# Kernel optimization log

Hardware: AMD Instinct MI355X
Metric: run time of the kernel (lower is better)

Reference implementation:

```python
import jax, jax.numpy as jnp
import numpy as np

D = 1024      # model_dim
H = 16        # num_heads
HD = D // H   # head_size
B = 4
S = 2048


def setup_inputs() -> dict:
    key = jax.random.key(0)
    ks = jax.random.split(key, 6)
    sc = 1.0 / np.sqrt(D)
    embedded = jax.random.normal(ks[0], (B, S, D), dtype=jnp.float32)
    # Per-head projection weights stacked: [H, D, HD] (nn.Linear, bias=False)
    Wq = jax.random.normal(ks[1], (H, D, HD), dtype=jnp.float32) * sc
    Wk = jax.random.normal(ks[2], (H, D, HD), dtype=jnp.float32) * sc
    Wv = jax.random.normal(ks[3], (H, D, HD), dtype=jnp.float32) * sc
    # Output projection nn.Linear(D, D) with bias
    Wo = jax.random.normal(ks[4], (D, D), dtype=jnp.float32) * sc
    bo = jax.random.normal(ks[5], (D,), dtype=jnp.float32) * sc
    return {"embedded": embedded, "Wq": Wq, "Wk": Wk, "Wv": Wv, "Wo": Wo, "bo": bo}


def reference(embedded, Wq, Wk, Wv, Wo, bo):
    # q,k,v: [B, H, S, HD]
    q = jnp.einsum('bsd,hde->bhse', embedded, Wq)
    k = jnp.einsum('bsd,hde->bhse', embedded, Wk)
    v = jnp.einsum('bsd,hde->bhse', embedded, Wv)
    scores = jnp.einsum('bhse,bhte->bhst', q, k) / jnp.sqrt(jnp.float32(HD))
    causal = jnp.tril(jnp.ones((S, S), dtype=bool))  # [S, S]
    scores = jnp.where(causal, scores, -jnp.inf)
    attn = jax.nn.softmax(scores, axis=-1)
    ctx = jnp.einsum('bhst,bhte->bhse', attn, v)  # [B, H, S, HD]
    # concat heads -> [B, S, D]
    concat = jnp.transpose(ctx, (0, 2, 1, 3)).reshape(B, S, D)
    # dropout=0.0 -> identity
    return concat @ Wo.T + bo
```

## Files before the change

### kernel.cpp

```cpp
#include <hip/hip_runtime.h>
#include <hip/hip_bf16.h>
#include <stdint.h>
#include <stddef.h>

typedef __bf16 bf16;
typedef __bf16 bf16x4 __attribute__((ext_vector_type(4)));
typedef __bf16 bf16x8 __attribute__((ext_vector_type(8)));
typedef float f32x4 __attribute__((ext_vector_type(4)));
typedef float f32x16 __attribute__((ext_vector_type(16)));


__device__ __forceinline__ void gload16(const void* g, void* lds) {
  __builtin_amdgcn_global_load_lds(
      (const __attribute__((address_space(1))) unsigned int*)(uintptr_t)g,
      (__attribute__((address_space(3))) unsigned int*)(unsigned int)(uintptr_t)lds,
      16, 0, 0);
}

__device__ __forceinline__ bf16x8 lds_read8(const bf16* base, int row, int slot) {
  const char* p = (const char*)base + row * 128 + ((slot ^ (row & 7)) << 4);
  return *(const bf16x8*)p;
}

__device__ __forceinline__ float f3max(float a, float b, float c) {
  return fmaxf(fmaxf(a, b), c);
}


__global__ void k_cvt_embed(const float* __restrict__ src, bf16* __restrict__ dst) {
  int i = blockIdx.x * blockDim.x + threadIdx.x;
  const float4* s4 = (const float4*)src;
  float4 a = s4[2 * i], b = s4[2 * i + 1];
  bf16x8 v;
  v[0] = (bf16)a.x; v[1] = (bf16)a.y; v[2] = (bf16)a.z; v[3] = (bf16)a.w;
  v[4] = (bf16)b.x; v[5] = (bf16)b.y; v[6] = (bf16)b.z; v[7] = (bf16)b.w;
  ((bf16x8*)dst)[i] = v;
}


__global__ void k_cvt_w(const float* __restrict__ Wq, const float* __restrict__ Wk,
                        const float* __restrict__ Wv, const float* __restrict__ Wo,
                        bf16* __restrict__ WT, bf16* __restrict__ WoB) {
  int i = blockIdx.x * blockDim.x + threadIdx.x;
  if (i < 16 * 192 * 1024) {
    int h = i / (192 * 1024);
    int rem = i - h * (192 * 1024);
    int r = rem >> 10;
    int d = rem & 1023;
    const float* W = (r < 64) ? Wq : (r < 128 ? Wk : Wv);
    int e = r & 63;
    WT[i] = (bf16)W[h * 65536 + d * 64 + e];
  } else {
    int j = i - 16 * 192 * 1024;
    WoB[j] = (bf16)Wo[j];
  }
}


__launch_bounds__(256, 2)
__global__ void k_qkv(const bf16* __restrict__ E, const bf16* __restrict__ WT,
                      bf16* __restrict__ Qo, bf16* __restrict__ Ko, bf16* __restrict__ Vt) {
  __shared__ __align__(16) bf16 As[128 * 64];
  __shared__ __align__(16) bf16 Bs[192 * 64];
  const int h = blockIdx.y;
  const int m0 = blockIdx.x * 128;
  const int tid = threadIdx.x;
  const int w = tid >> 6, lane = tid & 63;
  const int wm = w >> 1, wn = w & 1;
  const int cl = lane & 15, g4 = lane >> 4;
  const int srow = lane >> 3;
  const int scol = ((lane & 7) ^ (lane >> 3)) << 3;
  const bf16* Wh = WT + (size_t)h * 192 * 1024;
  f32x4 zero = {0.f, 0.f, 0.f, 0.f};
  f32x4 acc[4][6];
#pragma unroll
  for (int m = 0; m < 4; ++m)
#pragma unroll
    for (int n = 0; n < 6; ++n) acc[m][n] = zero;

  for (int kt = 0; kt < 16; ++kt) {
    const int k0 = kt * 64;
    __syncthreads();
#pragma unroll
    for (int c = 0; c < 4; ++c) {
      int cc = w * 4 + c;
      gload16(E + (size_t)(m0 + cc * 8 + srow) * 1024 + k0 + scol, (char*)As + cc * 1024);
    }
#pragma unroll
    for (int c = 0; c < 6; ++c) {
      int cc = w * 6 + c;
      gload16(Wh + (size_t)(cc * 8 + srow) * 1024 + k0 + scol, (char*)Bs + cc * 1024);
    }
    __syncthreads();
#pragma unroll
    for (int kk = 0; kk < 2; ++kk) {
      bf16x8 a[4], b[6];
#pragma unroll
      for (int m = 0; m < 4; ++m) a[m] = lds_read8(As, wm * 64 + m * 16 + cl, kk * 4 + g4);
#pragma unroll
      for (int n = 0; n < 6; ++n) b[n] = lds_read8(Bs, wn * 96 + n * 16 + cl, kk * 4 + g4);
#pragma unroll
      for (int m = 0; m < 4; ++m)
#pragma unroll
        for (int n = 0; n < 6; ++n)
          acc[m][n] = __builtin_amdgcn_mfma_f32_16x16x32_bf16(a[m], b[n], acc[m][n], 0, 0, 0);
    }
  }
#pragma unroll
  for (int n = 0; n < 6; ++n) {
    int ncol = wn * 96 + n * 16 + cl;
    int which = ncol >> 6, e = ncol & 63;
    if (which == 2) {
#pragma unroll
      for (int m = 0; m < 4; ++m) {
        int row = m0 + wm * 64 + m * 16 + g4 * 4;
        int bb = row >> 11, ss = row & 2047;
        bf16x4 vv;
#pragma unroll
        for (int r = 0; r < 4; ++r) vv[r] = (bf16)acc[m][n][r];
        *(bf16x4*)(Vt + ((size_t)(bb * 16 + h) * 64 + e) * 2048 + ss) = vv;
      }
    } else {
      bf16* dst = (which == 0) ? Qo : Ko;
      const float sc = (which == 0) ? 0.18033688f : 1.0f;
#pragma unroll
      for (int m = 0; m < 4; ++m) {
#pragma unroll
        for (int r = 0; r < 4; ++r) {
          int row = m0 + wm * 64 + m * 16 + g4 * 4 + r;
          int bb = row >> 11, ss = row & 2047;
          dst[(((size_t)(bb * 16 + h) * 2048 + ss) << 6) + e] = (bf16)(acc[m][n][r] * sc);
        }
      }
    }
  }
}


__launch_bounds__(512)
__global__ void k_attn(const bf16* __restrict__ Qg, const bf16* __restrict__ Kg,
                       const bf16* __restrict__ Vtg, bf16* __restrict__ CTX) {
  __shared__ __align__(16) bf16 KS[2][8192];
  __shared__ __align__(16) bf16 VT[2][8192];
  const int b = blockIdx.x;
  const int bh = b & 63;
  const int g = b >> 6;
  const int qt = (g < 4) ? g : 11 - g;
  const int q0 = qt * 256;
  const int tid = threadIdx.x, w = tid >> 6, lane = tid & 63;
  const int ql = lane & 31, hi = lane >> 5;
  const int q = q0 + 32 * w + ql;
  const int qmin = q0 + 32 * w;
  const int qmax = qmin + 31;
  const bf16* Qb = Qg + (size_t)bh * (2048 * 64);
  const bf16* Kb = Kg + (size_t)bh * (2048 * 64);
  const bf16* Vb = Vtg + (size_t)bh * (64 * 2048);
  const int ntk = 2 * qt + 2;

  bf16x8 qf[4];
#pragma unroll
  for (int ks = 0; ks < 4; ++ks)
    qf[ks] = *(const bf16x8*)(Qb + (size_t)q * 64 + ks * 16 + hi * 8);

  f32x16 o0, o1;
#pragma unroll
  for (int i = 0; i < 16; ++i) { o0[i] = 0.f; o1[i] = 0.f; }
  float mr = -1e30f, ls = 0.f;

  const int srowK = w * 8 + (lane >> 3);
  const int phiRow = (srowK & ~12) | ((srowK & 4) << 1) | ((srowK & 8) >> 1);
  const int scolK = ((lane & 7) ^ ((lane >> 3) & 7)) << 3;
  const int vrow0 = w * 4 + (lane >> 4);
  const int vkey0 = ((lane & 15) ^ (vrow0 & 7)) * 8;
  const int vrow1 = 32 + vrow0;
  const int vkey1 = ((lane & 15) ^ (vrow1 & 7)) * 8;
  int offs[4];
#pragma unroll
  for (int ks = 0; ks < 4; ++ks) offs[ks] = (ks * 32 + hi * 16) ^ ((ql & 7) << 4);

  auto stage = [&](int kv, int buf) {
    gload16(Kb + (size_t)(kv + phiRow) * 64 + scolK, (char*)KS[buf] + w * 1024);
    gload16(Kb + (size_t)(kv + 64 + phiRow) * 64 + scolK, (char*)KS[buf] + 8192 + w * 1024);
    gload16(Vb + (size_t)vrow0 * 2048 + kv + vkey0, (char*)VT[buf] + w * 1024);
    gload16(Vb + (size_t)vrow1 * 2048 + kv + vkey1, (char*)VT[buf] + 8192 + w * 1024);
  };

  auto do_half = [&](int kv0h, const char* kbase, const char* vtb, int halfB) {
    f32x16 s0, s1;
#pragma unroll
    for (int i = 0; i < 16; ++i) { s0[i] = 0.f; s1[i] = 0.f; }
    __builtin_amdgcn_s_setprio(1);
#pragma unroll
    for (int ks = 0; ks < 4; ++ks) {
      bf16x8 k0 = *(const bf16x8*)(kbase + ql * 128 + offs[ks]);
      bf16x8 k1 = *(const bf16x8*)(kbase + (32 + ql) * 128 + offs[ks]);
      s0 = __builtin_amdgcn_mfma_f32_32x32x16_bf16(k0, qf[ks], s0, 0, 0, 0);
      s1 = __builtin_amdgcn_mfma_f32_32x32x16_bf16(k1, qf[ks], s1, 0, 0, 0);
    }
    __builtin_amdgcn_s_setprio(0);
    if (kv0h + 63 > qmin) {
      int dqh = q - kv0h - 8 * hi;
#pragma unroll
      for (int r = 0; r < 16; ++r) {
        const int c0 = (r & 7) + ((r & 8) << 1);
        if (c0 > dqh) s0[r] = -1e30f;
        if (c0 + 32 > dqh) s1[r] = -1e30f;
      }
    }
    float x0 = f3max(s0[0], s0[1], s0[2]);
    float x1 = f3max(s0[3], s0[4], s0[5]);
    float x2 = f3max(s0[6], s0[7], s0[8]);
    float x3 = f3max(s0[9], s0[10], s0[11]);
    float x4 = f3max(s0[12], s0[13], s0[14]);
    float x5 = f3max(s0[15], s1[0], s1[1]);
    float x6 = f3max(s1[2], s1[3], s1[4]);
    float x7 = f3max(s1[5], s1[6], s1[7]);
    float x8 = f3max(s1[8], s1[9], s1[10]);
    float x9 = f3max(s1[11], s1[12], s1[13]);
    float xa = fmaxf(s1[14], s1[15]);
    float y0 = f3max(x0, x1, x2);
    float y1 = f3max(x3, x4, x5);
    float y2 = f3max(x6, x7, x8);
    float y3 = fmaxf(x9, xa);
    float pmax = f3max(y0, y1, fmaxf(y2, y3));
    pmax = fmaxf(pmax, __shfl_xor(pmax, 32));
    if (__any(pmax - mr > 8.0f)) {
      float mnew = fmaxf(mr, pmax);
      float al = exp2f(mr - mnew);
      mr = mnew; ls *= al;
#pragma unroll
      for (int i = 0; i < 16; ++i) { o0[i] *= al; o1[i] *= al; }
    }
#pragma unroll
    for (int i = 0; i < 16; ++i) {
      s0[i] = exp2f(s0[i] - mr);
      s1[i] = exp2f(s1[i] - mr);
    }
    float a8[8];
#pragma unroll
    for (int i = 0; i < 8; ++i) a8[i] = (s0[i] + s0[i + 8]) + (s1[i] + s1[i + 8]);
    float rs = ((a8[0] + a8[1]) + (a8[2] + a8[3])) + ((a8[4] + a8[5]) + (a8[6] + a8[7]));
    rs += __shfl_xor(rs, 32);
    ls += rs;
    bf16x8 pf[4];
#pragma unroll
    for (int j = 0; j < 8; ++j) {
      pf[0][j] = (bf16)s0[j];
      pf[1][j] = (bf16)s0[8 + j];
      pf[2][j] = (bf16)s1[j];
      pf[3][j] = (bf16)s1[8 + j];
    }
    __builtin_amdgcn_s_setprio(1);
#pragma unroll
    for (int ks = 0; ks < 4; ++ks) {
      bf16x8 v0 = *(const bf16x8*)(vtb + ql * 256 + halfB + offs[ks]);
      bf16x8 v1 = *(const bf16x8*)(vtb + (32 + ql) * 256 + halfB + offs[ks]);
      o0 = __builtin_amdgcn_mfma_f32_32x32x16_bf16(v0, pf[ks], o0, 0, 0, 0);
      o1 = __builtin_amdgcn_mfma_f32_32x32x16_bf16(v1, pf[ks], o1, 0, 0, 0);
    }
    __builtin_amdgcn_s_setprio(0);
  };

  stage(0, 0);

  int cur = 0;
  for (int t = 0; t < ntk; ++t) {
    const int kv0 = t * 128;
    __syncthreads();
    if (t + 1 < ntk) stage(kv0 + 128, cur ^ 1);
    if (kv0 <= qmax)
      do_half(kv0, (const char*)KS[cur], (const char*)VT[cur], 0);
    if (kv0 + 64 <= qmax)
      do_half(kv0 + 64, (const char*)KS[cur] + 8192, (const char*)VT[cur], 128);
    cur ^= 1;
  }

  const float inv = 1.0f / ls;
  const int bb = bh >> 4, hh = bh & 15;
  bf16* Cp = CTX + ((size_t)(bb * 2048 + q) * 1024) + hh * 64;
#pragma unroll
  for (int r = 0; r < 16; ++r) {
    int d0 = (r & 3) + 8 * (r >> 2) + 4 * hi;
    Cp[d0] = (bf16)(o0[r] * inv);
    Cp[32 + d0] = (bf16)(o1[r] * inv);
  }
}


__launch_bounds__(256, 2)
__global__ void k_oproj(const bf16* __restrict__ X, const bf16* __restrict__ Wb,
                        const float* __restrict__ bo, float* __restrict__ out) {
  __shared__ __align__(16) bf16 As[128 * 64];
  __shared__ __align__(16) bf16 Bs[128 * 64];
  const int m0 = blockIdx.x * 128, n0 = blockIdx.y * 128;
  const int tid = threadIdx.x, w = tid >> 6, lane = tid & 63;
  const int wm = w >> 1, wn = w & 1;
  const int cl = lane & 15, g4 = lane >> 4;
  const int srow = lane >> 3;
  const int scol = ((lane & 7) ^ (lane >> 3)) << 3;
  f32x4 zero = {0.f, 0.f, 0.f, 0.f};
  f32x4 acc[4][4];
#pragma unroll
  for (int m = 0; m < 4; ++m)
#pragma unroll
    for (int n = 0; n < 4; ++n) acc[m][n] = zero;

  for (int kt = 0; kt < 16; ++kt) {
    const int k0 = kt * 64;
    __syncthreads();
#pragma unroll
    for (int c = 0; c < 4; ++c) {
      int cc = w * 4 + c;
      gload16(X + (size_t)(m0 + cc * 8 + srow) * 1024 + k0 + scol, (char*)As + cc * 1024);
      gload16(Wb + (size_t)(n0 + cc * 8 + srow) * 1024 + k0 + scol, (char*)Bs + cc * 1024);
    }
    __syncthreads();
#pragma unroll
    for (int kk = 0; kk < 2; ++kk) {
      bf16x8 a[4], b[4];
#pragma unroll
      for (int m = 0; m < 4; ++m) a[m] = lds_read8(As, wm * 64 + m * 16 + cl, kk * 4 + g4);
#pragma unroll
      for (int n = 0; n < 4; ++n) b[n] = lds_read8(Bs, wn * 64 + n * 16 + cl, kk * 4 + g4);
#pragma unroll
      for (int m = 0; m < 4; ++m)
#pragma unroll
        for (int n = 0; n < 4; ++n)
          acc[m][n] = __builtin_amdgcn_mfma_f32_16x16x32_bf16(a[m], b[n], acc[m][n], 0, 0, 0);
    }
  }
#pragma unroll
  for (int n = 0; n < 4; ++n) {
    int col = n0 + wn * 64 + n * 16 + cl;
    float bias = bo[col];
#pragma unroll
    for (int m = 0; m < 4; ++m)
#pragma unroll
      for (int r = 0; r < 4; ++r) {
        int row = m0 + wm * 64 + m * 16 + g4 * 4 + r;
        out[(size_t)row * 1024 + col] = acc[m][n][r] + bias;
      }
  }
}


extern "C" void kernel_launch(void* const* d_in, const int* in_sizes, int n_in,
                              void* d_out, int out_size, void* d_ws, size_t ws_size,
                              hipStream_t stream) {
  const float* emb = (const float*)d_in[0];
  const float* Wq  = (const float*)d_in[1];
  const float* Wk  = (const float*)d_in[2];
  const float* Wv  = (const float*)d_in[3];
  const float* Wo  = (const float*)d_in[4];
  const float* bo  = (const float*)d_in[5];
  float* out = (float*)d_out;

  const size_t NEED = (size_t)72 << 20;
  if (ws_size < NEED) return;

  char* ws = (char*)d_ws;
  bf16* E   = (bf16*)(ws);
  bf16* WT  = (bf16*)(ws + ((size_t)16 << 20));
  bf16* WoB = (bf16*)(ws + ((size_t)22 << 20));
  bf16* Qw  = (bf16*)(ws + ((size_t)24 << 20));
  bf16* Kw  = (bf16*)(ws + ((size_t)40 << 20));
  bf16* Vtw = (bf16*)(ws + ((size_t)56 << 20));
  bf16* CTX = E;

  k_cvt_embed<<<4096, 256, 0, stream>>>(emb, E);
  k_cvt_w<<<16384, 256, 0, stream>>>(Wq, Wk, Wv, Wo, WT, WoB);
  k_qkv<<<dim3(64, 16), 256, 0, stream>>>(E, WT, Qw, Kw, Vtw);
  k_attn<<<512, 512, 0, stream>>>(Qw, Kw, Vtw, CTX);
  k_oproj<<<dim3(64, 8), 256, 0, stream>>>(CTX, WoB, bo, out);
}
```

Before: 170.6 us.

## Double-buffer LDS tiles in QKV and output-projection GEMMs; reorder QKV grid

Both GEMM kernels now keep two LDS buffers per operand. The next K-tile's global-to-LDS loads are issued right after the barrier, so they run while MFMA works on the current tile, and the loop needs only one barrier per iteration instead of two. The QKV grid is transposed so heads vary fastest, which lets blocks sharing the same embedding rows run close together and reuse them in L2. LDS use doubles (80KB per QKV block), which leaves little headroom for two blocks per CU.

Measured after the change: 162.4 us. 4.8% less time.

```diff
diff --git a/kernel.cpp b/kernel.cpp
--- a/kernel.cpp
+++ b/kernel.cpp
@@ -60,10 +60,10 @@
 __launch_bounds__(256, 2)
 __global__ void k_qkv(const bf16* __restrict__ E, const bf16* __restrict__ WT,
                       bf16* __restrict__ Qo, bf16* __restrict__ Ko, bf16* __restrict__ Vt) {
-  __shared__ __align__(16) bf16 As[128 * 64];
-  __shared__ __align__(16) bf16 Bs[192 * 64];
-  const int h = blockIdx.y;
-  const int m0 = blockIdx.x * 128;
+  __shared__ __align__(16) bf16 As[2][128 * 64];
+  __shared__ __align__(16) bf16 Bs[2][192 * 64];
+  const int h = blockIdx.x;
+  const int m0 = blockIdx.y * 128;
   const int tid = threadIdx.x;
   const int w = tid >> 6, lane = tid & 63;
   const int wm = w >> 1, wn = w & 1;
@@ -78,33 +78,39 @@
 #pragma unroll
     for (int n = 0; n < 6; ++n) acc[m][n] = zero;
 
-  for (int kt = 0; kt < 16; ++kt) {
+  auto stage = [&](int kt, int buf) {
     const int k0 = kt * 64;
-    __syncthreads();
 #pragma unroll
     for (int c = 0; c < 4; ++c) {
       int cc = w * 4 + c;
-      gload16(E + (size_t)(m0 + cc * 8 + srow) * 1024 + k0 + scol, (char*)As + cc * 1024);
+      gload16(E + (size_t)(m0 + cc * 8 + srow) * 1024 + k0 + scol, (char*)As[buf] + cc * 1024);
     }
 #pragma unroll
     for (int c = 0; c < 6; ++c) {
       int cc = w * 6 + c;
-      gload16(Wh + (size_t)(cc * 8 + srow) * 1024 + k0 + scol, (char*)Bs + cc * 1024);
-    }
+      gload16(Wh + (size_t)(cc * 8 + srow) * 1024 + k0 + scol, (char*)Bs[buf] + cc * 1024);
+    }
+  };
+
+  stage(0, 0);
+  int cur = 0;
+  for (int kt = 0; kt < 16; ++kt) {
     __syncthreads();
+    if (kt + 1 < 16) stage(kt + 1, cur ^ 1);
 #pragma unroll
     for (int kk = 0; kk < 2; ++kk) {
       bf16x8 a[4], b[6];
 #pragma unroll
-      for (int m = 0; m < 4; ++m) a[m] = lds_read8(As, wm * 64 + m * 16 + cl, kk * 4 + g4);
-#pragma unroll
-      for (int n = 0; n < 6; ++n) b[n] = lds_read8(Bs, wn * 96 + n * 16 + cl, kk * 4 + g4);
+      for (int m = 0; m < 4; ++m) a[m] = lds_read8(As[cur], wm * 64 + m * 16 + cl, kk * 4 + g4);
+#pragma unroll
+      for (int n = 0; n < 6; ++n) b[n] = lds_read8(Bs[cur], wn * 96 + n * 16 + cl, kk * 4 + g4);
 #pragma unroll
       for (int m = 0; m < 4; ++m)
 #pragma unroll
         for (int n = 0; n < 6; ++n)
           acc[m][n] = __builtin_amdgcn_mfma_f32_16x16x32_bf16(a[m], b[n], acc[m][n], 0, 0, 0);
     }
+    cur ^= 1;
   }
 #pragma unroll
   for (int n = 0; n < 6; ++n) {
@@ -290,8 +296,8 @@
 __launch_bounds__(256, 2)
 __global__ void k_oproj(const bf16* __restrict__ X, const bf16* __restrict__ Wb,
                         const float* __restrict__ bo, float* __restrict__ out) {
-  __shared__ __align__(16) bf16 As[128 * 64];
-  __shared__ __align__(16) bf16 Bs[128 * 64];
+  __shared__ __align__(16) bf16 As[2][128 * 64];
+  __shared__ __align__(16) bf16 Bs[2][128 * 64];
   const int m0 = blockIdx.x * 128, n0 = blockIdx.y * 128;
   const int tid = threadIdx.x, w = tid >> 6, lane = tid & 63;
   const int wm = w >> 1, wn = w & 1;
@@ -305,29 +311,35 @@
 #pragma unroll
     for (int n = 0; n < 4; ++n) acc[m][n] = zero;
 
-  for (int kt = 0; kt < 16; ++kt) {
+  auto stage = [&](int kt, int buf) {
     const int k0 = kt * 64;
-    __syncthreads();
 #pragma unroll
     for (int c = 0; c < 4; ++c) {
       int cc = w * 4 + c;
-      gload16(X + (size_t)(m0 + cc * 8 + srow) * 1024 + k0 + scol, (char*)As + cc * 1024);
-      gload16(Wb + (size_t)(n0 + cc * 8 + srow) * 1024 + k0 + scol, (char*)Bs + cc * 1024);
-    }
+      gload16(X + (size_t)(m0 + cc * 8 + srow) * 1024 + k0 + scol, (char*)As[buf] + cc * 1024);
+      gload16(Wb + (size_t)(n0 + cc * 8 + srow) * 1024 + k0 + scol, (char*)Bs[buf] + cc * 1024);
+    }
+  };
+
+  stage(0, 0);
+  int cur = 0;
+  for (int kt = 0; kt < 16; ++kt) {
     __syncthreads();
+    if (kt + 1 < 16) stage(kt + 1, cur ^ 1);
 #pragma unroll
     for (int kk = 0; kk < 2; ++kk) {
       bf16x8 a[4], b[4];
 #pragma unroll
-      for (int m = 0; m < 4; ++m) a[m] = lds_read8(As, wm * 64 + m * 16 + cl, kk * 4 + g4);
-#pragma unroll
-      for (int n = 0; n < 4; ++n) b[n] = lds_read8(Bs, wn * 64 + n * 16 + cl, kk * 4 + g4);
+      for (int m = 0; m < 4; ++m) a[m] = lds_read8(As[cur], wm * 64 + m * 16 + cl, kk * 4 + g4);
+#pragma unroll
+      for (int n = 0; n < 4; ++n) b[n] = lds_read8(Bs[cur], wn * 64 + n * 16 + cl, kk * 4 + g4);
 #pragma unroll
       for (int m = 0; m < 4; ++m)
 #pragma unroll
         for (int n = 0; n < 4; ++n)
           acc[m][n] = __builtin_amdgcn_mfma_f32_16x16x32_bf16(a[m], b[n], acc[m][n], 0, 0, 0);
     }
+    cur ^= 1;
   }
 #pragma unroll
   for (int n = 0; n < 4; ++n) {
@@ -369,7 +381,7 @@
 
   k_cvt_embed<<<4096, 256, 0, stream>>>(emb, E);
   k_cvt_w<<<16384, 256, 0, stream>>>(Wq, Wk, Wv, Wo, WT, WoB);
-  k_qkv<<<dim3(64, 16), 256, 0, stream>>>(E, WT, Qw, Kw, Vtw);
+  k_qkv<<<dim3(16, 64), 256, 0, stream>>>(E, WT, Qw, Kw, Vtw);
   k_attn<<<512, 512, 0, stream>>>(Qw, Kw, Vtw, CTX);
   k_oproj<<<dim3(64, 8), 256, 0, stream>>>(CTX, WoB, bo, out);
 }
```
